# Performance work log

Hardware: AMD Instinct MI355X
Metric: run time of the kernel (lower is better)

The kernel has to match this reference:

```python
import jax, jax.numpy as jnp
import numpy as np

NUM_ATTRS = 8    # A: number of attribute names in attr_map
NUM_VALS = 16    # V: number of distinct values per attribute


def setup_inputs() -> dict:
    key = jax.random.key(0)
    k1, k2 = jax.random.split(key)
    B, D = 2_000_000, 8
    predictions = jax.random.normal(k1, (B, D), dtype=jnp.float32)
    attr_vals = jax.random.randint(k2, (B, NUM_ATTRS), 0, NUM_VALS, dtype=jnp.int32)
    return {"predictions": predictions, "attr_vals": attr_vals}


def reference(predictions, attr_vals):
    B, A = attr_vals.shape
    V = NUM_VALS
    # per-node mean of sigmoid probs; stacking rows then .mean() == mean of per-node means
    per_node = jnp.mean(jax.nn.sigmoid(predictions), axis=1)  # [B]
    # flatten (attr, value) groups into A*V segments
    seg_ids = (attr_vals + jnp.arange(A, dtype=attr_vals.dtype)[None, :] * V).reshape(-1)  # [B*A]
    vals = jnp.broadcast_to(per_node[:, None], (B, A)).reshape(-1)  # [B*A]
    sums = jax.ops.segment_sum(vals, seg_ids, num_segments=A * V)
    counts = jax.ops.segment_sum(jnp.ones_like(vals), seg_ids, num_segments=A * V)
    means = (sums / jnp.maximum(counts, 1.0)).reshape(A, V)      # [A, V]
    present = (counts > 0).reshape(A, V)                          # [A, V]
    # pairwise squared diffs of group means within each attribute (i < j)
    diff = means[:, :, None] - means[:, None, :]                  # [A, V, V]
    triu = jnp.triu(jnp.ones((V, V), dtype=bool), k=1)
    pair_mask = present[:, :, None] & present[:, None, :] & triu[None, :, :]
    total_loss = jnp.sum(jnp.where(pair_mask, diff * diff, 0.0))
    num_comparisons = jnp.sum(pair_mask)
    return jnp.where(num_comparisons > 0, total_loss / num_comparisons, 0.0)
```

## Files before the change

### kernel.cpp

```cpp
#include <hip/hip_runtime.h>

#define NA 8
#define NV 16
#define NS (NA * NV)
#define NP 4
#define NJ 256
#define NE (NP * NJ)
#define FIX_SHIFT 43
#define FIX_MASK ((1ULL << FIX_SHIFT) - 1)
#define FIX_SCALE 2147483648.0f

__global__ __launch_bounds__(256) void k1_accum(
    const float* __restrict__ preds,
    const int*   __restrict__ attrs,
    unsigned long long* __restrict__ partials,
    int B, int nb)
{
    __shared__ unsigned long long h[NE];
    for (int i = threadIdx.x; i < NE; i += 256) h[i] = 0ULL;
    __syncthreads();

    const int stride = nb * 256;
    for (int r = blockIdx.x * 256 + threadIdx.x; r < B; r += stride) {
        const float4* p4 = (const float4*)(preds + (size_t)r * NA);
        float4 p0 = p4[0];
        float4 p1 = p4[1];

        float s = __builtin_amdgcn_rcpf(1.0f + __expf(-p0.x))
                + __builtin_amdgcn_rcpf(1.0f + __expf(-p0.y))
                + __builtin_amdgcn_rcpf(1.0f + __expf(-p0.z))
                + __builtin_amdgcn_rcpf(1.0f + __expf(-p0.w))
                + __builtin_amdgcn_rcpf(1.0f + __expf(-p1.x))
                + __builtin_amdgcn_rcpf(1.0f + __expf(-p1.y))
                + __builtin_amdgcn_rcpf(1.0f + __expf(-p1.z))
                + __builtin_amdgcn_rcpf(1.0f + __expf(-p1.w));
        float per_node = s * 0.125f;
        unsigned int fixed = (unsigned int)(per_node * FIX_SCALE);
        unsigned long long add = (1ULL << FIX_SHIFT) | (unsigned long long)fixed;

        const int4* a4 = (const int4*)(attrs + (size_t)r * NA);
        int4 a0 = a4[0];
        int4 a1 = a4[1];

        atomicAdd(&h[0 * NJ + ((a0.x << 4) | a0.y)], add);
        atomicAdd(&h[1 * NJ + ((a0.z << 4) | a0.w)], add);
        atomicAdd(&h[2 * NJ + ((a1.x << 4) | a1.y)], add);
        atomicAdd(&h[3 * NJ + ((a1.z << 4) | a1.w)], add);
    }
    __syncthreads();

    unsigned long long* dst = partials + (size_t)blockIdx.x * NE;
    for (int i = threadIdx.x; i < NE; i += 256) {
        dst[i] = h[i];
    }
}

__global__ __launch_bounds__(256) void k2_reduce(
    const unsigned long long* __restrict__ partials,
    unsigned long long* __restrict__ jsum,
    unsigned int*       __restrict__ jcnt,
    int nb)
{
    const int e = blockIdx.x;
    unsigned long long sum = 0ULL;
    unsigned int cnt = 0u;
    for (int b = threadIdx.x; b < nb; b += 256) {
        unsigned long long p = partials[(size_t)b * NE + e];
        cnt += (unsigned int)(p >> FIX_SHIFT);
        sum += (p & FIX_MASK);
    }
    for (int off = 32; off > 0; off >>= 1) {
        sum += __shfl_down(sum, off, 64);
        cnt += __shfl_down(cnt, off, 64);
    }
    __shared__ unsigned long long ws_[4];
    __shared__ unsigned int wc_[4];
    const int wave = threadIdx.x >> 6;
    if ((threadIdx.x & 63) == 0) { ws_[wave] = sum; wc_[wave] = cnt; }
    __syncthreads();
    if (threadIdx.x == 0) {
        jsum[e] = ws_[0] + ws_[1] + ws_[2] + ws_[3];
        jcnt[e] = wc_[0] + wc_[1] + wc_[2] + wc_[3];
    }
}

__global__ __launch_bounds__(128) void k3_finalize(
    const unsigned long long* __restrict__ jsum,
    const unsigned int*       __restrict__ jcnt,
    float* __restrict__ out)
{
    __shared__ double s_mean[NS];
    __shared__ int    s_pres[NS];

    const int t = threadIdx.x;
    const int a = t >> 4;
    const int v = t & (NV - 1);
    const int p = a >> 1;

    unsigned long long S = 0ULL;
    unsigned int C = 0u;
    if ((a & 1) == 0) {
        for (int j = 0; j < NV; ++j) {
            const int e = p * NJ + (v << 4) + j;
            S += jsum[e]; C += jcnt[e];
        }
    } else {
        for (int i = 0; i < NV; ++i) {
            const int e = p * NJ + (i << 4) + v;
            S += jsum[e]; C += jcnt[e];
        }
    }
    s_pres[t] = (C > 0u) ? 1 : 0;
    s_mean[t] = (C > 0u)
        ? ((double)S * (1.0 / (double)FIX_SCALE)) / (double)C : 0.0;
    __syncthreads();

    double loss = 0.0;
    int    ncmp = 0;
    if (s_pres[t]) {
        const double mi = s_mean[t];
        for (int j = v + 1; j < NV; ++j) {
            const int sj = (a << 4) + j;
            if (s_pres[sj]) {
                const double d = mi - s_mean[sj];
                loss += d * d;
                ncmp += 1;
            }
        }
    }
    for (int off = 32; off > 0; off >>= 1) {
        loss += __shfl_down(loss, off, 64);
        ncmp += __shfl_down(ncmp, off, 64);
    }
    __shared__ double w_loss[2];
    __shared__ int    w_ncmp[2];
    const int wave = t >> 6;
    if ((t & 63) == 0) { w_loss[wave] = loss; w_ncmp[wave] = ncmp; }
    __syncthreads();
    if (t == 0) {
        const double total = w_loss[0] + w_loss[1];
        const int    n     = w_ncmp[0] + w_ncmp[1];
        out[0] = (n > 0) ? (float)(total / (double)n) : 0.0f;
    }
}

extern "C" void kernel_launch(void* const* d_in, const int* in_sizes, int n_in,
                              void* d_out, int out_size, void* d_ws, size_t ws_size,
                              hipStream_t stream) {
    const float* preds = (const float*)d_in[0];
    const int*   attrs = (const int*)d_in[1];
    float*       out   = (float*)d_out;

    const int B = in_sizes[1] / NA;

    const size_t tail = (size_t)NE * (sizeof(unsigned long long) + sizeof(unsigned int));
    int nb = 1024;
    while (nb > 256 &&
           (size_t)NE * nb * sizeof(unsigned long long) + tail > ws_size) {
        nb >>= 1;
    }

    unsigned long long* partials = (unsigned long long*)d_ws;
    unsigned long long* jsum = (unsigned long long*)((char*)d_ws +
        (size_t)NE * nb * sizeof(unsigned long long));
    unsigned int* jcnt = (unsigned int*)(jsum + NE);

    k1_accum<<<nb, 256, 0, stream>>>(preds, attrs, partials, B, nb);
    k2_reduce<<<NE, 256, 0, stream>>>(partials, jsum, jcnt, nb);
    k3_finalize<<<1, 128, 0, stream>>>(jsum, jcnt, out);
}
```

Measured before the change: 159.5 us.

## Split rows across thread pairs and use two-level coalesced partial reduction

Each row is now handled by two adjacent threads, each loading one float4 of predictions and one int4 of attributes. The thread pair combines its two sigmoid sums through a lane shuffle and each thread does two of the row's four shared-memory atomics. The partial-histogram reduction is split into two kernels: one sums groups of 8 blocks with coalesced contiguous reads, and a second sums those results per element. The default block count rises to 2048, which adds a kernel launch and more workspace traffic in exchange for better load coalescing and more parallelism.

```diff
diff --git a/kernel.cpp b/kernel.cpp
--- a/kernel.cpp
+++ b/kernel.cpp
@@ -11,41 +11,31 @@
 #define FIX_SCALE 2147483648.0f
 
 __global__ __launch_bounds__(256) void k1_accum(
-    const float* __restrict__ preds,
-    const int*   __restrict__ attrs,
+    const float4* __restrict__ preds4,
+    const int4*   __restrict__ attrs4,
     unsigned long long* __restrict__ partials,
-    int B, int nb)
+    int total4, int nb)
 {
     __shared__ unsigned long long h[NE];
     for (int i = threadIdx.x; i < NE; i += 256) h[i] = 0ULL;
     __syncthreads();
 
+    const int pbase = (threadIdx.x & 1) ? 2 * NJ : 0;
     const int stride = nb * 256;
-    for (int r = blockIdx.x * 256 + threadIdx.x; r < B; r += stride) {
-        const float4* p4 = (const float4*)(preds + (size_t)r * NA);
-        float4 p0 = p4[0];
-        float4 p1 = p4[1];
+    for (int idx = blockIdx.x * 256 + threadIdx.x; idx < total4; idx += stride) {
+        float4 p = preds4[idx];
+        int4   a = attrs4[idx];
 
-        float s = __builtin_amdgcn_rcpf(1.0f + __expf(-p0.x))
-                + __builtin_amdgcn_rcpf(1.0f + __expf(-p0.y))
-                + __builtin_amdgcn_rcpf(1.0f + __expf(-p0.z))
-                + __builtin_amdgcn_rcpf(1.0f + __expf(-p0.w))
-                + __builtin_amdgcn_rcpf(1.0f + __expf(-p1.x))
-                + __builtin_amdgcn_rcpf(1.0f + __expf(-p1.y))
-                + __builtin_amdgcn_rcpf(1.0f + __expf(-p1.z))
-                + __builtin_amdgcn_rcpf(1.0f + __expf(-p1.w));
-        float per_node = s * 0.125f;
+        float half = __builtin_amdgcn_rcpf(1.0f + __expf(-p.x))
+                   + __builtin_amdgcn_rcpf(1.0f + __expf(-p.y))
+                   + __builtin_amdgcn_rcpf(1.0f + __expf(-p.z))
+                   + __builtin_amdgcn_rcpf(1.0f + __expf(-p.w));
+        float per_node = (half + __shfl_xor(half, 1)) * 0.125f;
         unsigned int fixed = (unsigned int)(per_node * FIX_SCALE);
         unsigned long long add = (1ULL << FIX_SHIFT) | (unsigned long long)fixed;
 
-        const int4* a4 = (const int4*)(attrs + (size_t)r * NA);
-        int4 a0 = a4[0];
-        int4 a1 = a4[1];
-
-        atomicAdd(&h[0 * NJ + ((a0.x << 4) | a0.y)], add);
-        atomicAdd(&h[1 * NJ + ((a0.z << 4) | a0.w)], add);
-        atomicAdd(&h[2 * NJ + ((a1.x << 4) | a1.y)], add);
-        atomicAdd(&h[3 * NJ + ((a1.z << 4) | a1.w)], add);
+        atomicAdd(&h[pbase + ((a.x << 4) | a.y)], add);
+        atomicAdd(&h[pbase + NJ + ((a.z << 4) | a.w)], add);
     }
     __syncthreads();
 
@@ -55,33 +45,49 @@
     }
 }
 
-__global__ __launch_bounds__(256) void k2_reduce(
+__global__ __launch_bounds__(256) void k2a_reduce(
     const unsigned long long* __restrict__ partials,
+    unsigned long long* __restrict__ p2sum,
+    unsigned int*       __restrict__ p2cnt,
+    int g)
+{
+    const unsigned long long* src = partials + (size_t)blockIdx.x * g * NE;
+    unsigned long long s0 = 0, s1 = 0, s2 = 0, s3 = 0;
+    unsigned int c0 = 0, c1 = 0, c2 = 0, c3 = 0;
+    for (int b = 0; b < g; ++b) {
+        const unsigned long long* s = src + (size_t)b * NE;
+        unsigned long long p0 = s[threadIdx.x];
+        unsigned long long p1 = s[threadIdx.x + 256];
+        unsigned long long p2 = s[threadIdx.x + 512];
+        unsigned long long p3 = s[threadIdx.x + 768];
+        s0 += p0 & FIX_MASK; c0 += (unsigned int)(p0 >> FIX_SHIFT);
+        s1 += p1 & FIX_MASK; c1 += (unsigned int)(p1 >> FIX_SHIFT);
+        s2 += p2 & FIX_MASK; c2 += (unsigned int)(p2 >> FIX_SHIFT);
+        s3 += p3 & FIX_MASK; c3 += (unsigned int)(p3 >> FIX_SHIFT);
+    }
+    unsigned long long* ds = p2sum + (size_t)blockIdx.x * NE;
+    unsigned int*       dc = p2cnt + (size_t)blockIdx.x * NE;
+    ds[threadIdx.x] = s0; ds[threadIdx.x + 256] = s1;
+    ds[threadIdx.x + 512] = s2; ds[threadIdx.x + 768] = s3;
+    dc[threadIdx.x] = c0; dc[threadIdx.x + 256] = c1;
+    dc[threadIdx.x + 512] = c2; dc[threadIdx.x + 768] = c3;
+}
+
+__global__ __launch_bounds__(64) void k2b_reduce(
+    const unsigned long long* __restrict__ p2sum,
+    const unsigned int*       __restrict__ p2cnt,
     unsigned long long* __restrict__ jsum,
     unsigned int*       __restrict__ jcnt,
-    int nb)
+    int n2)
 {
-    const int e = blockIdx.x;
-    unsigned long long sum = 0ULL;
-    unsigned int cnt = 0u;
-    for (int b = threadIdx.x; b < nb; b += 256) {
-        unsigned long long p = partials[(size_t)b * NE + e];
-        cnt += (unsigned int)(p >> FIX_SHIFT);
-        sum += (p & FIX_MASK);
+    const int e = blockIdx.x * 64 + threadIdx.x;
+    unsigned long long S = 0; unsigned int C = 0;
+    for (int j = 0; j < n2; ++j) {
+        S += p2sum[(size_t)j * NE + e];
+        C += p2cnt[(size_t)j * NE + e];
     }
-    for (int off = 32; off > 0; off >>= 1) {
-        sum += __shfl_down(sum, off, 64);
-        cnt += __shfl_down(cnt, off, 64);
-    }
-    __shared__ unsigned long long ws_[4];
-    __shared__ unsigned int wc_[4];
-    const int wave = threadIdx.x >> 6;
-    if ((threadIdx.x & 63) == 0) { ws_[wave] = sum; wc_[wave] = cnt; }
-    __syncthreads();
-    if (threadIdx.x == 0) {
-        jsum[e] = ws_[0] + ws_[1] + ws_[2] + ws_[3];
-        jcnt[e] = wc_[0] + wc_[1] + wc_[2] + wc_[3];
-    }
+    jsum[e] = S;
+    jcnt[e] = C;
 }
 
 __global__ __launch_bounds__(128) void k3_finalize(
@@ -147,25 +153,29 @@
 extern "C" void kernel_launch(void* const* d_in, const int* in_sizes, int n_in,
                               void* d_out, int out_size, void* d_ws, size_t ws_size,
                               hipStream_t stream) {
-    const float* preds = (const float*)d_in[0];
-    const int*   attrs = (const int*)d_in[1];
-    float*       out   = (float*)d_out;
+    const float4* preds4 = (const float4*)d_in[0];
+    const int4*   attrs4 = (const int4*)d_in[1];
+    float*        out    = (float*)d_out;
 
     const int B = in_sizes[1] / NA;
+    const int total4 = B * 2;
 
-    const size_t tail = (size_t)NE * (sizeof(unsigned long long) + sizeof(unsigned int));
-    int nb = 1024;
-    while (nb > 256 &&
-           (size_t)NE * nb * sizeof(unsigned long long) + tail > ws_size) {
-        nb >>= 1;
-    }
+    auto need = [](int nb) -> size_t {
+        int n2 = nb / 8;
+        return (size_t)nb * NE * 8 + (size_t)n2 * NE * 12 + (size_t)NE * 12;
+    };
+    int nb = 2048;
+    while (nb > 256 && need(nb) > ws_size) nb >>= 1;
+    const int n2 = nb / 8;
 
     unsigned long long* partials = (unsigned long long*)d_ws;
-    unsigned long long* jsum = (unsigned long long*)((char*)d_ws +
-        (size_t)NE * nb * sizeof(unsigned long long));
-    unsigned int* jcnt = (unsigned int*)(jsum + NE);
+    unsigned long long* p2sum = partials + (size_t)nb * NE;
+    unsigned int*       p2cnt = (unsigned int*)(p2sum + (size_t)n2 * NE);
+    unsigned long long* jsum  = (unsigned long long*)(p2cnt + (size_t)n2 * NE);
+    unsigned int*       jcnt  = (unsigned int*)(jsum + NE);
 
-    k1_accum<<<nb, 256, 0, stream>>>(preds, attrs, partials, B, nb);
-    k2_reduce<<<NE, 256, 0, stream>>>(partials, jsum, jcnt, nb);
+    k1_accum<<<nb, 256, 0, stream>>>(preds4, attrs4, partials, total4, nb);
+    k2a_reduce<<<n2, 256, 0, stream>>>(partials, p2sum, p2cnt, 8);
+    k2b_reduce<<<NE / 64, 64, 0, stream>>>(p2sum, p2cnt, jsum, jcnt, n2);
     k3_finalize<<<1, 128, 0, stream>>>(jsum, jcnt, out);
 }
```

Result: slower. 222.6 us (+39.6%).
